# Optimization experiments

Measured on AMD Instinct MI355X. Metric: run time of the kernel, lower is better.

## Reference

```python
import jax, jax.numpy as jnp
import numpy as np

WS = 7   # window_size
SS = 3   # shift_size = window_size // 2
NH = 16  # num_heads


def _rel_pos_index(ws):
    coords = np.stack(np.meshgrid(np.arange(ws), np.arange(ws), indexing='ij'))  # (2, ws, ws)
    cf = coords.reshape(2, -1)
    rel = (cf[:, :, None] - cf[:, None, :]).transpose(1, 2, 0)
    rel[:, :, 0] += ws - 1
    rel[:, :, 1] += ws - 1
    rel[:, :, 0] *= 2 * ws - 1
    return rel.sum(-1)  # (ws*ws, ws*ws) int

REL_IDX = _rel_pos_index(WS)


def _attn_mask(h, w, ws, ss):
    img = np.zeros((h, w))
    sls = (slice(0, -ws), slice(-ws, -ss), slice(-ss, None))
    cnt = 0
    for i in sls:
        for j in sls:
            img[i, j] = cnt
            cnt += 1
    mw = img.reshape(h // ws, ws, w // ws, ws).transpose(0, 2, 1, 3).reshape(-1, ws * ws)
    d = mw[:, None, :] - mw[:, :, None]  # (nW, N, N)
    return np.where(d != 0, -100.0, 0.0).astype(np.float32)


def _part(x, ws):
    b, h, w, c = x.shape
    return x.reshape(b, h // ws, ws, w // ws, ws, c).transpose(0, 1, 3, 2, 4, 5).reshape(-1, ws * ws, c)


def _rev(win, ws, h, w):
    c = win.shape[-1]
    b = win.shape[0] // ((h // ws) * (w // ws))
    return win.reshape(b, h // ws, w // ws, ws, ws, c).transpose(0, 1, 3, 2, 4, 5).reshape(b, h, w, c)


def _ln(x, g, b):
    m = x.mean(-1, keepdims=True)
    v = x.var(-1, keepdims=True)
    return (x - m) / jnp.sqrt(v + 1e-5) * g + b


def _wattn(x, qkv_w, qkv_b, proj_w, proj_b, table, mask):
    B_, N, C = x.shape
    hd = C // NH
    scale = hd ** -0.5
    qkv = (x @ qkv_w.T + qkv_b).reshape(B_, N, 3, NH, hd).transpose(2, 0, 3, 1, 4)
    q, k, v = qkv[0] * scale, qkv[1], qkv[2]  # (B_, NH, N, hd)
    attn = jnp.einsum('bhnd,bhmd->bhnm', q, k)
    bias = table[REL_IDX.reshape(-1)].reshape(N, N, NH).transpose(2, 0, 1)  # (NH, N, N)
    attn = attn + bias[None]
    if mask is not None:
        nW = mask.shape[0]
        attn = (attn.reshape(B_ // nW, nW, NH, N, N) + mask[None, :, None]).reshape(B_, NH, N, N)
    attn = jax.nn.softmax(attn, axis=-1)
    out = jnp.einsum('bhnm,bhmd->bhnd', attn, v).transpose(0, 2, 1, 3).reshape(B_, N, C)
    return out @ proj_w.T + proj_b


def _mlp(x, w1, b1, w2, b2):
    return jax.nn.gelu(x @ w1.T + b1, approximate=False) @ w2.T + b2


def _forward(x, w_norm1_g, w_norm1_b, w_qkv_w, w_qkv_b, w_proj_w, w_proj_b, w_table,
             w_norm2_g, w_norm2_b, w_fc1_w, w_fc1_b, w_fc2_w, w_fc2_b,
             sw_norm1_g, sw_norm1_b, sw_qkv_w, sw_qkv_b, sw_proj_w, sw_proj_b, sw_table,
             sw_norm2_g, sw_norm2_b, sw_fc1_w, sw_fc1_b, sw_fc2_w, sw_fc2_b):
    b, c, h, w = x.shape
    x = jnp.transpose(x, (0, 2, 3, 1)).reshape(b, h * w, c)  # (B, HW, C)
    shortcut = x
    xn = _ln(x, w_norm1_g, w_norm1_b).reshape(b, h, w, c)
    aw = _wattn(_part(xn, WS), w_qkv_w, w_qkv_b, w_proj_w, w_proj_b, w_table, None)
    x = shortcut + _rev(aw, WS, h, w).reshape(b, h * w, c)
    x = x + _mlp(_ln(x, w_norm2_g, w_norm2_b), w_fc1_w, w_fc1_b, w_fc2_w, w_fc2_b)
    # shifted-window branch (shift_size > 0 since min(h,w) > window_size)
    xn = _ln(x, sw_norm1_g, sw_norm1_b)
    mask = jnp.asarray(_attn_mask(h, w, WS, SS))
    shifted = jnp.roll(xn.reshape(b, h, w, c), (-SS, -SS), axis=(1, 2))
    sa = _wattn(_part(shifted, WS), sw_qkv_w, sw_qkv_b, sw_proj_w, sw_proj_b, sw_table, mask)
    shifted = jnp.roll(_rev(sa, WS, h, w), (SS, SS), axis=(1, 2)).reshape(b, h * w, c)
    # NOTE: source adds the residual to the *normalized* activations here; kept faithful.
    x = xn + shifted
    x = x + _mlp(_ln(x, sw_norm2_g, sw_norm2_b), sw_fc1_w, sw_fc1_b, sw_fc2_w, sw_fc2_b)
    return x.reshape(b, h, w, c)


def setup_inputs() -> dict:
    key = jax.random.key(0)
    ks = jax.random.split(key, 32)
    B, C, H, W = 8, 512, 56, 56
    Cm = 4 * C
    T = (2 * WS - 1) ** 2

    def rn(k, shape, s=0.02):
        return jax.random.normal(k, shape, jnp.float32) * s

    d = {'x': jax.random.normal(ks[0], (B, C, H, W), jnp.float32)}
    for i, p in enumerate(['w', 'sw']):
        o = 1 + i * 6
        d[p + '_norm1_g'] = jnp.ones((C,), jnp.float32)
        d[p + '_norm1_b'] = jnp.zeros((C,), jnp.float32)
        d[p + '_qkv_w'] = rn(ks[o], (3 * C, C))
        d[p + '_qkv_b'] = jnp.zeros((3 * C,), jnp.float32)
        d[p + '_proj_w'] = rn(ks[o + 1], (C, C))
        d[p + '_proj_b'] = jnp.zeros((C,), jnp.float32)
        d[p + '_table'] = rn(ks[o + 2], (T, NH))
        d[p + '_norm2_g'] = jnp.ones((C,), jnp.float32)
        d[p + '_norm2_b'] = jnp.zeros((C,), jnp.float32)
        d[p + '_fc1_w'] = rn(ks[o + 3], (Cm, C))
        d[p + '_fc1_b'] = jnp.zeros((Cm,), jnp.float32)
        d[p + '_fc2_w'] = rn(ks[o + 4], (C, Cm))
        d[p + '_fc2_b'] = jnp.zeros((C,), jnp.float32)
    return d


def reference(x, w_norm1_g, w_norm1_b, w_qkv_w, w_qkv_b, w_proj_w, w_proj_b, w_table,
              w_norm2_g, w_norm2_b, w_fc1_w, w_fc1_b, w_fc2_w, w_fc2_b,
              sw_norm1_g, sw_norm1_b, sw_qkv_w, sw_qkv_b, sw_proj_w, sw_proj_b, sw_table,
              sw_norm2_g, sw_norm2_b, sw_fc1_w, sw_fc1_b, sw_fc2_w, sw_fc2_b):
    return _forward(x, w_norm1_g, w_norm1_b, w_qkv_w, w_qkv_b, w_proj_w, w_proj_b, w_table,
                    w_norm2_g, w_norm2_b, w_fc1_w, w_fc1_b, w_fc2_w, w_fc2_b,
                    sw_norm1_g, sw_norm1_b, sw_qkv_w, sw_qkv_b, sw_proj_w, sw_proj_b, sw_table,
                    sw_norm2_g, sw_norm2_b, sw_fc1_w, sw_fc1_b, sw_fc2_w, sw_fc2_b)
```

## Files before the change

### kernel.cpp

```cpp
#include <hip/hip_runtime.h>
#include <hip/hip_bf16.h>

using bf16 = __hip_bfloat16;

#define B_      8
#define C_      512
#define H_      56
#define W_      56
#define HW_     3136
#define M_      25088
#define NH_     16
#define HD_     32
#define WS_     7
#define NT_     49

typedef __attribute__((ext_vector_type(8))) short bf16x8;
typedef __attribute__((ext_vector_type(4))) float f32x4;

#define AS1(p) ((const __attribute__((address_space(1))) void*)(p))
#define AS3(p) ((__attribute__((address_space(3))) void*)(p))

__device__ inline float bf2f(const bf16 v) {
    unsigned short u = *reinterpret_cast<const unsigned short*>(&v);
    return __uint_as_float((unsigned)u << 16);
}
__device__ inline unsigned short f2bfu(float f) {
    bf16 h = __float2bfloat16(f);
    return *reinterpret_cast<unsigned short*>(&h);
}
__device__ inline float rdv(const float* p) { return *p; }
__device__ inline float rdv(const bf16* p)  { return bf2f(*p); }
__device__ inline void stv(float* p, float v) { *p = v; }
__device__ inline void stv(bf16* p, float v)  { *p = __float2bfloat16(v); }

__device__ inline float gelu_t(float v) {
    const float u = v * (0.79788456080286536f + 0.035677408136300125f * v * v);
    const float e = __expf(2.0f * u);
    return 0.5f * v * (2.0f - 2.0f / (e + 1.0f));
}

__global__ void k_detect(const void* g1, int* flag) {
    const unsigned short* u = (const unsigned short*)g1;
    *flag = (u[0] == 0x3F80u) ? 1 : 0;
}

struct WArgs {
    const void* src[26];
    bf16*       dst[26];
    int         n[26];
};
__global__ __launch_bounds__(256) void k_convert_all(WArgs a, const int* flag) {
    const int isb = *flag;
    const int gid = blockIdx.x * 256 + threadIdx.x;
    const int stride = gridDim.x * 256;
    #pragma unroll 1
    for (int w = 0; w < 26; ++w) {
        const int n = a.n[w];
        bf16* d = a.dst[w];
        if (isb) {
            const unsigned short* s = (const unsigned short*)a.src[w];
            for (int i = gid; i < n; i += stride) ((unsigned short*)d)[i] = s[i];
        } else {
            const float* s = (const float*)a.src[w];
            for (int i = gid; i < n; i += stride) d[i] = __float2bfloat16(s[i]);
        }
    }
}

__global__ __launch_bounds__(256) void k_transpose_in(const void* xin, bf16* X,
                                                      const int* flag) {
    __shared__ float tile[32][33];
    const int isb = *flag;
    const int p0 = blockIdx.x * 32, c0 = blockIdx.y * 32, b = blockIdx.z;
    const int tp = threadIdx.x & 31, tc = threadIdx.x >> 5;
    const size_t ibase = (size_t)b * C_ * HW_;
    #pragma unroll
    for (int i = 0; i < 4; ++i) {
        const int c = tc + i * 8;
        const size_t idx = ibase + (size_t)(c0 + c) * HW_ + p0 + tp;
        tile[c][tp] = isb ? bf2f(((const bf16*)xin)[idx]) : ((const float*)xin)[idx];
    }
    __syncthreads();
    const int wc = threadIdx.x & 31, wp = threadIdx.x >> 5;
    bf16* dst = X + (size_t)b * HW_ * C_;
    #pragma unroll
    for (int i = 0; i < 4; ++i) {
        const int p = wp + i * 8;
        dst[(size_t)(p0 + p) * C_ + c0 + wc] = __float2bfloat16(tile[wc][p]);
    }
}

__global__ __launch_bounds__(128) void k_layernorm(const bf16* __restrict__ X,
                                                   const bf16* __restrict__ g,
                                                   const bf16* __restrict__ bta,
                                                   bf16* __restrict__ XN) {
    const int tok = blockIdx.x;
    const ushort4 u = reinterpret_cast<const ushort4*>(X + (size_t)tok * C_)[threadIdx.x];
    float4 v;
    v.x = __uint_as_float((unsigned)u.x << 16);
    v.y = __uint_as_float((unsigned)u.y << 16);
    v.z = __uint_as_float((unsigned)u.z << 16);
    v.w = __uint_as_float((unsigned)u.w << 16);
    float s  = v.x + v.y + v.z + v.w;
    float s2 = v.x * v.x + v.y * v.y + v.z * v.z + v.w * v.w;
    #pragma unroll
    for (int o = 32; o > 0; o >>= 1) { s += __shfl_down(s, o); s2 += __shfl_down(s2, o); }
    __shared__ float sh[4];
    if ((threadIdx.x & 63) == 0) { sh[threadIdx.x >> 6] = s; sh[2 + (threadIdx.x >> 6)] = s2; }
    __syncthreads();
    const float ts = sh[0] + sh[1], ts2 = sh[2] + sh[3];
    const float m = ts * (1.0f / C_);
    const float var = ts2 * (1.0f / C_) - m * m;
    const float r = rsqrtf(var + 1e-5f);
    const int c = threadIdx.x * 4;
    ushort4 o;
    o.x = f2bfu((v.x - m) * r * bf2f(g[c + 0]) + bf2f(bta[c + 0]));
    o.y = f2bfu((v.y - m) * r * bf2f(g[c + 1]) + bf2f(bta[c + 1]));
    o.z = f2bfu((v.z - m) * r * bf2f(g[c + 2]) + bf2f(bta[c + 2]));
    o.w = f2bfu((v.w - m) * r * bf2f(g[c + 3]) + bf2f(bta[c + 3]));
    reinterpret_cast<ushort4*>(XN + (size_t)tok * C_)[threadIdx.x] = o;
}

template <typename TADD, typename TO, bool GELU, bool ADD, bool FINAL>
__global__ __launch_bounds__(512, 2) void k_gemm_mfma(const bf16* __restrict__ A,
                                                      const bf16* __restrict__ Wt,
                                                      const bf16* __restrict__ bias,
                                                      const TADD* __restrict__ addp,
                                                      TO* __restrict__ out,
                                                      const int* flag,
                                                      int N, int K) {
    __shared__ bf16 sA[3][256 * 64];
    __shared__ bf16 sB[3][128 * 64];
    const int tid  = threadIdx.x;
    const int lane = tid & 63;
    const int wid  = tid >> 6;
    const int wr   = wid >> 1;
    const int wc2  = wid & 1;

    const int nwg  = gridDim.x;
    const int orig = blockIdx.x;
    const int nx = nwg >> 3, rr_ = nwg & 7;
    const int xcd = orig & 7, offw = orig >> 3;
    const int wg = (xcd < rr_ ? xcd * (nx + 1) : rr_ * (nx + 1) + (xcd - rr_) * nx) + offw;
    const int gx = N >> 7;
    const int m0 = (wg / gx) * 256, n0 = (wg % gx) * 128;

    const f32x4 vz = {0.f, 0.f, 0.f, 0.f};
    f32x4 acc[4][4];
    #pragma unroll
    for (int i = 0; i < 4; ++i)
        #pragma unroll
        for (int j = 0; j < 4; ++j) acc[i][j] = vz;

    const int sr8  = lane >> 3;
    const int schk = (lane & 7) ^ sr8;
    const bf16* gA0 = A  + (size_t)(m0 + sr8) * K + schk * 8;
    const bf16* gB0 = Wt + (size_t)(n0 + sr8) * K + schk * 8;

    const int l15 = lane & 15, g4 = lane >> 4;
    const int NTLE = K >> 6;

    #pragma unroll
    for (int tt = 0; tt < 3; ++tt) {
        const int kt = tt << 6;
        #pragma unroll
        for (int p = 0; p < 4; ++p) {
            const int q = wid * 4 + p;
            __builtin_amdgcn_global_load_lds(AS1(gA0 + (size_t)(q * 8) * K + kt),
                                             AS3(&sA[tt][q * 512]), 16, 0, 0);
        }
        #pragma unroll
        for (int p = 0; p < 2; ++p) {
            const int q = wid * 2 + p;
            __builtin_amdgcn_global_load_lds(AS1(gB0 + (size_t)(q * 8) * K + kt),
                                             AS3(&sB[tt][q * 512]), 16, 0, 0);
        }
    }

    for (int t = 0; t < NTLE; ++t) {
        const int rem = NTLE - 1 - t;
        if (rem >= 2)      asm volatile("s_waitcnt vmcnt(12)" ::: "memory");
        else if (rem == 1) asm volatile("s_waitcnt vmcnt(6)"  ::: "memory");
        else               asm volatile("s_waitcnt vmcnt(0)"  ::: "memory");
        __builtin_amdgcn_s_barrier();

        const int buf = t % 3;
        bf16x8 bfr[4][2];
        #pragma unroll
        for (int ks = 0; ks < 2; ++ks) {
            const int ch = ((ks << 2) | g4) ^ (l15 & 7);
            #pragma unroll
            for (int j = 0; j < 4; ++j) {
                const int rowB = wc2 * 64 + j * 16 + l15;
                bfr[j][ks] = *reinterpret_cast<const bf16x8*>(&sB[buf][rowB * 64 + ch * 8]);
            }
        }
        const int ch0 = g4 ^ (l15 & 7);
        const int ch1 = (4 | g4) ^ (l15 & 7);
        __builtin_amdgcn_s_setprio(1);
        #pragma unroll
        for (int i = 0; i < 4; ++i) {
            const int rowA = wr * 64 + i * 16 + l15;
            const bf16x8 a0 = *reinterpret_cast<const bf16x8*>(&sA[buf][rowA * 64 + ch0 * 8]);
            const bf16x8 a1 = *reinterpret_cast<const bf16x8*>(&sA[buf][rowA * 64 + ch1 * 8]);
            #pragma unroll
            for (int j = 0; j < 4; ++j) {
                acc[i][j] = __builtin_amdgcn_mfma_f32_16x16x32_bf16(a0, bfr[j][0], acc[i][j], 0, 0, 0);
                acc[i][j] = __builtin_amdgcn_mfma_f32_16x16x32_bf16(a1, bfr[j][1], acc[i][j], 0, 0, 0);
            }
        }
        __builtin_amdgcn_s_setprio(0);

        asm volatile("s_waitcnt lgkmcnt(0)" ::: "memory");
        __builtin_amdgcn_s_barrier();

        const int tn = t + 3;
        if (tn < NTLE) {
            const int kt = tn << 6;
            #pragma unroll
            for (int p = 0; p < 4; ++p) {
                const int q = wid * 4 + p;
                __builtin_amdgcn_global_load_lds(AS1(gA0 + (size_t)(q * 8) * K + kt),
                                                 AS3(&sA[buf][q * 512]), 16, 0, 0);
            }
            #pragma unroll
            for (int p = 0; p < 2; ++p) {
                const int q = wid * 2 + p;
                __builtin_amdgcn_global_load_lds(AS1(gB0 + (size_t)(q * 8) * K + kt),
                                                 AS3(&sB[buf][q * 512]), 16, 0, 0);
            }
        }
    }

    int obf = 0;
    if constexpr (FINAL) obf = *flag;
    const int colBase = n0 + wc2 * 64 + l15;
    const int rowTop  = m0 + wr * 64 + g4 * 4;
    float bc[4];
    #pragma unroll
    for (int j = 0; j < 4; ++j) bc[j] = bf2f(bias[colBase + j * 16]);
    #pragma unroll
    for (int i = 0; i < 4; ++i) {
        #pragma unroll
        for (int r = 0; r < 4; ++r) {
            const int row = rowTop + i * 16 + r;
            #pragma unroll
            for (int j = 0; j < 4; ++j) {
                const int col = colBase + j * 16;
                float v = acc[i][j][r] + bc[j];
                if constexpr (GELU) v = gelu_t(v);
                if constexpr (ADD)  v += rdv(&addp[(size_t)row * N + col]);
                if constexpr (FINAL) {
                    if (obf) ((bf16*)(void*)out)[(size_t)row * N + col] = __float2bfloat16(v);
                    else     ((float*)(void*)out)[(size_t)row * N + col] = v;
                } else {
                    stv(&out[(size_t)row * N + col], v);
                }
            }
        }
    }
}

__global__ __launch_bounds__(256) void k_mktbl(const bf16* __restrict__ table,
                                               bf16* __restrict__ out, int shifted) {
    const int bh = blockIdx.x;
    const int cls = bh >> 4, h = bh & 15;
    const int rowE = shifted ? (cls >> 1) : 0;
    const int colE = shifted ? (cls & 1) : 0;
    for (int e = threadIdx.x; e < 64 * 64; e += 256) {
        const int i = e >> 6, j = e & 63;
        float v;
        if (i < NT_ && j < NT_) {
            const int yi = i / WS_, xi = i % WS_, yj = j / WS_, xj = j % WS_;
            const int ridx = (yi - yj + 6) * 13 + (xi - xj + 6);
            v = bf2f(table[ridx * NH_ + h]);
            const int ri = (rowE ? (yi < 4 ? 1 : 2) : 0) * 3 + (colE ? (xi < 4 ? 1 : 2) : 0);
            const int rj = (rowE ? (yj < 4 ? 1 : 2) : 0) * 3 + (colE ? (xj < 4 ? 1 : 2) : 0);
            if (ri != rj) v -= 100.f;
        } else if (j >= NT_) {
            v = -3e30f;
        } else {
            v = 0.f;
        }
        out[((size_t)bh << 12) + e] = __float2bfloat16(v);
    }
}

template <int SS, bool SHIFTED>
__global__ __launch_bounds__(64) void k_attn_mfma(const bf16* __restrict__ QKV,
                                                  const bf16* __restrict__ tbl,
                                                  bf16* __restrict__ O) {
    __shared__ __align__(16) short uQK[5120];
    __shared__ __align__(16) short uVt[2304];
    __shared__ int toks[NT_];
    short* Qs = uQK;
    short* Ks = uQK + 2560;
    short* Ps = uQK;

    const int lane = threadIdx.x;
    const int head = blockIdx.x & 15;
    const int win  = blockIdx.x >> 4;
    const int bl = win >> 6, w64 = win & 63;
    const int wy = w64 >> 3, wx = w64 & 7;

    if (lane < NT_) {
        const int dy = lane / WS_, dx = lane % WS_;
        const int sr = wy * WS_ + dy, scn = wx * WS_ + dx;
        const int r = (sr + SS) % H_, c = (scn + SS) % W_;
        toks[lane] = bl * HW_ + r * W_ + c;
    }
    __syncthreads();

    const int g4 = lane >> 4, l15 = lane & 15;
    const int tsg = lane >> 2, csg = (lane & 3) * 8;

    #pragma unroll
    for (int rr = 0; rr < 4; ++rr) {
        const int t = rr * 16 + tsg;
        bf16x8 qv = {0,0,0,0,0,0,0,0}, kv = {0,0,0,0,0,0,0,0}, vv = {0,0,0,0,0,0,0,0};
        if (t < NT_) {
            const bf16* base = QKV + (size_t)toks[t] * 1536 + head * HD_ + csg;
            qv = *reinterpret_cast<const bf16x8*>(base);
            kv = *reinterpret_cast<const bf16x8*>(base + 512);
            vv = *reinterpret_cast<const bf16x8*>(base + 1024);
        }
        *reinterpret_cast<bf16x8*>(&Qs[t * 40 + csg]) = qv;
        *reinterpret_cast<bf16x8*>(&Ks[t * 40 + csg]) = kv;
        #pragma unroll
        for (int e = 0; e < 8; ++e) uVt[(csg + e) * 72 + t] = ((const short*)&vv)[e];
    }
    __syncthreads();

    bf16x8 aq[4], bk[4];
    #pragma unroll
    for (int f = 0; f < 4; ++f) {
        aq[f] = *reinterpret_cast<const bf16x8*>(&Qs[(f * 16 + l15) * 40 + g4 * 8]);
        bk[f] = *reinterpret_cast<const bf16x8*>(&Ks[(f * 16 + l15) * 40 + g4 * 8]);
    }
    const f32x4 vz = {0.f, 0.f, 0.f, 0.f};
    f32x4 sacc[4][4];
    #pragma unroll
    for (int qi = 0; qi < 4; ++qi)
        #pragma unroll
        for (int kj = 0; kj < 4; ++kj)
            sacc[qi][kj] = __builtin_amdgcn_mfma_f32_16x16x32_bf16(aq[qi], bk[kj], vz, 0, 0, 0);
    __syncthreads();

    const int cls = SHIFTED ? (((wy == 7) ? 2 : 0) + ((wx == 7) ? 1 : 0)) : 0;
    const bf16* tb = tbl + (((size_t)(cls * NH_ + head)) << 12);
    const float scale = 0.17677669529663687f;
    #pragma unroll
    for (int qi = 0; qi < 4; ++qi) {
        #pragma unroll
        for (int r = 0; r < 4; ++r) {
            const int i = qi * 16 + g4 * 4 + r;
            const bf16* trow = tb + (i << 6);
            float sv[4];
            #pragma unroll
            for (int kj = 0; kj < 4; ++kj)
                sv[kj] = sacc[qi][kj][r] * scale + bf2f(trow[kj * 16 + l15]);
            float mx = fmaxf(fmaxf(sv[0], sv[1]), fmaxf(sv[2], sv[3]));
            #pragma unroll
            for (int d = 1; d <= 8; d <<= 1) mx = fmaxf(mx, __shfl_xor(mx, d));
            float p[4], sum = 0.f;
            #pragma unroll
            for (int kj = 0; kj < 4; ++kj) { p[kj] = __expf(sv[kj] - mx); sum += p[kj]; }
            #pragma unroll
            for (int d = 1; d <= 8; d <<= 1) sum += __shfl_xor(sum, d);
            const float inv = 1.0f / sum;
            #pragma unroll
            for (int kj = 0; kj < 4; ++kj)
                Ps[i * 72 + kj * 16 + l15] = (short)f2bfu(p[kj] * inv);
        }
    }
    __syncthreads();

    f32x4 oacc[4][2];
    #pragma unroll
    for (int qi = 0; qi < 4; ++qi) { oacc[qi][0] = vz; oacc[qi][1] = vz; }
    #pragma unroll
    for (int ks = 0; ks < 2; ++ks) {
        bf16x8 bv[2];
        #pragma unroll
        for (int dj = 0; dj < 2; ++dj)
            bv[dj] = *reinterpret_cast<const bf16x8*>(&uVt[(dj * 16 + l15) * 72 + ks * 32 + g4 * 8]);
        #pragma unroll
        for (int qi = 0; qi < 4; ++qi) {
            const bf16x8 ap = *reinterpret_cast<const bf16x8*>(&Ps[(qi * 16 + l15) * 72 + ks * 32 + g4 * 8]);
            #pragma unroll
            for (int dj = 0; dj < 2; ++dj)
                oacc[qi][dj] = __builtin_amdgcn_mfma_f32_16x16x32_bf16(ap, bv[dj], oacc[qi][dj], 0, 0, 0);
        }
    }
    #pragma unroll
    for (int qi = 0; qi < 4; ++qi) {
        #pragma unroll
        for (int r = 0; r < 4; ++r) {
            const int i = qi * 16 + g4 * 4 + r;
            if (i < NT_) {
                const size_t ob = (size_t)toks[i] * C_ + head * HD_ + l15;
                O[ob]      = __float2bfloat16(oacc[qi][0][r]);
                O[ob + 16] = __float2bfloat16(oacc[qi][1][r]);
            }
        }
    }
}

extern "C" void kernel_launch(void* const* d_in, const int* in_sizes, int n_in,
                              void* d_out, int out_size, void* d_ws, size_t ws_size,
                              hipStream_t stream) {
    (void)out_size; (void)ws_size;
    char* ws = (char*)d_ws;
    const size_t WEIGHT_RESERVE = 12651520;
    bf16*  WC   = (bf16*)ws;
    int*   FLG  = (int*)(ws + WEIGHT_RESERVE);
    bf16*  TBL1 = (bf16*)(ws + WEIGHT_RESERVE + 1024);
    bf16*  TBL2 = (bf16*)(ws + WEIGHT_RESERVE + 1024 + 131072);
    bf16*  X    = (bf16*)(ws + WEIGHT_RESERVE + 656384);
    bf16*  XN   = X + (size_t)M_ * C_;
    char*  BIG  = (char*)(XN + (size_t)M_ * C_);

    size_t offs[27];
    size_t off = 0;
    for (int i = 1; i < n_in && i < 27; ++i) { offs[i] = off; off += (size_t)((in_sizes[i] + 7) & ~7); }
    auto wc = [&](int i) { return (const bf16*)(WC + offs[i]); };

    k_detect<<<1, 1, 0, stream>>>(d_in[1], FLG);
    {
        WArgs a;
        for (int i = 1; i < 27; ++i) {
            a.src[i - 1] = d_in[i];
            a.dst[i - 1] = WC + offs[i];
            a.n[i - 1]   = in_sizes[i];
        }
        k_convert_all<<<512, 256, 0, stream>>>(a, FLG);
    }
    k_mktbl<<<16, 256, 0, stream>>>(wc(7),  TBL1, 0);
    k_mktbl<<<64, 256, 0, stream>>>(wc(20), TBL2, 1);

    const dim3 gT(HW_ / 32, C_ / 32, B_);
    k_transpose_in<<<gT, 256, 0, stream>>>(d_in[0], X, FLG);

    bf16* QKV = (bf16*)BIG;
    bf16* ATT = (bf16*)(BIG + (size_t)M_ * 1536 * 2);
    bf16* HID = (bf16*)BIG;

    const int gQ = (1536 / 128) * (M_ / 256);
    const int gP = (512 / 128)  * (M_ / 256);
    const int gF = (2048 / 128) * (M_ / 256);
    const dim3 gA(B_ * 64 * NH_);

    k_layernorm<<<M_, 128, 0, stream>>>(X, wc(1), wc(2), XN);
    k_gemm_mfma<bf16, bf16, false, false, false><<<gQ, 512, 0, stream>>>(
        XN, wc(3), wc(4), (const bf16*)nullptr, QKV, nullptr, 1536, C_);
    k_attn_mfma<0, false><<<gA, 64, 0, stream>>>(QKV, TBL1, ATT);
    k_gemm_mfma<bf16, bf16, false, true, false><<<gP, 512, 0, stream>>>(
        ATT, wc(5), wc(6), X, X, nullptr, C_, C_);
    k_layernorm<<<M_, 128, 0, stream>>>(X, wc(8), wc(9), XN);
    k_gemm_mfma<bf16, bf16, true, false, false><<<gF, 512, 0, stream>>>(
        XN, wc(10), wc(11), (const bf16*)nullptr, HID, nullptr, 2048, C_);
    k_gemm_mfma<bf16, bf16, false, true, false><<<gP, 512, 0, stream>>>(
        HID, wc(12), wc(13), X, X, nullptr, C_, 2048);
    k_layernorm<<<M_, 128, 0, stream>>>(X, wc(14), wc(15), XN);
    k_gemm_mfma<bf16, bf16, false, false, false><<<gQ, 512, 0, stream>>>(
        XN, wc(16), wc(17), (const bf16*)nullptr, QKV, nullptr, 1536, C_);
    k_attn_mfma<3, true><<<gA, 64, 0, stream>>>(QKV, TBL2, ATT);
    k_gemm_mfma<bf16, bf16, false, true, false><<<gP, 512, 0, stream>>>(
        ATT, wc(18), wc(19), XN, X, nullptr, C_, C_);
    k_layernorm<<<M_, 128, 0, stream>>>(X, wc(21), wc(22), XN);
    k_gemm_mfma<bf16, bf16, true, false, false><<<gF, 512, 0, stream>>>(
        XN, wc(23), wc(24), (const bf16*)nullptr, HID, nullptr, 2048, C_);
    k_gemm_mfma<bf16, float, false, true, true><<<gP, 512, 0, stream>>>(
        HID, wc(25), wc(26), X, (float*)d_out, FLG, C_, 2048);
}
```

Measured before the change: 849.3 us.

## Add 256x256-tile MFMA GEMM with XCD-aware block remap for QKV and MLP

Adds a new GEMM kernel that computes 256x256 output tiles with 8 waves, double-buffered half-tiles loaded straight into LDS, interleaved prefetch across the k-loop, and setprio around the MFMA bursts. Workgroup ids are remapped so consecutive tiles land on the same XCD, which should improve L2 reuse. The kernel replaces the older 256x128 GEMM for the QKV, FC1 and FC2 projections, raising arithmetic intensity per loaded byte. The cost is more registers and LDS per block and fewer blocks for the N=512 GEMMs, which may hurt occupancy or load balance.

```diff
diff --git a/kernel.cpp b/kernel.cpp
--- a/kernel.cpp
+++ b/kernel.cpp
@@ -119,6 +119,168 @@
     o.z = f2bfu((v.z - m) * r * bf2f(g[c + 2]) + bf2f(bta[c + 2]));
     o.w = f2bfu((v.w - m) * r * bf2f(g[c + 3]) + bf2f(bta[c + 3]));
     reinterpret_cast<ushort4*>(XN + (size_t)tok * C_)[threadIdx.x] = o;
+}
+
+template <typename TADD, typename TO, bool GELU, bool ADD, bool FINAL>
+__global__ __launch_bounds__(512, 2) void k_gemm8(const bf16* __restrict__ A,
+                                                  const bf16* __restrict__ Wt,
+                                                  const bf16* __restrict__ bias,
+                                                  const TADD* __restrict__ addp,
+                                                  TO* __restrict__ out,
+                                                  const int* flag,
+                                                  int N, int K) {
+    __shared__ bf16 sA[2][2][128 * 64];
+    __shared__ bf16 sB[2][2][128 * 64];
+    const int tid  = threadIdx.x;
+    const int lane = tid & 63;
+    const int wid  = tid >> 6;
+    const int wr   = wid >> 2;
+    const int wc2  = wid & 3;
+    const int bh   = wc2 >> 1;
+    const int brl  = (wc2 & 1) * 64;
+
+    const int nwg  = gridDim.x;
+    const int orig = blockIdx.x;
+    const int nx = nwg >> 3, rr_ = nwg & 7;
+    const int xcd = orig & 7, offw = orig >> 3;
+    const int wg = (xcd < rr_ ? xcd * (nx + 1) : rr_ * (nx + 1) + (xcd - rr_) * nx) + offw;
+    const int gx = N >> 8;
+    const int m0 = (wg / gx) * 256, n0 = (wg % gx) * 256;
+
+    const f32x4 vz = {0.f, 0.f, 0.f, 0.f};
+    f32x4 acc[8][4];
+    #pragma unroll
+    for (int i = 0; i < 8; ++i)
+        #pragma unroll
+        for (int j = 0; j < 4; ++j) acc[i][j] = vz;
+
+    const int sr8  = lane >> 3;
+    const int schk = (lane & 7) ^ sr8;
+    const bf16* gA0 = A  + (size_t)(m0 + sr8) * K + schk * 8;
+    const bf16* gB0 = Wt + (size_t)(n0 + sr8) * K + schk * 8;
+
+    const int l15 = lane & 15, g4 = lane >> 4;
+    const int NTL = K >> 6;
+    const int NITER = NTL >> 1;
+
+    auto stageA = [&](int d, int h, int T) {
+        const int kt = T << 6;
+        #pragma unroll
+        for (int p = 0; p < 2; ++p) {
+            const int q = wid * 2 + p;
+            __builtin_amdgcn_global_load_lds(
+                AS1(gA0 + (size_t)(h * 128 + q * 8) * K + kt),
+                AS3(&sA[d][h][q * 512]), 16, 0, 0);
+        }
+    };
+    auto stageB = [&](int d, int h, int T) {
+        const int kt = T << 6;
+        #pragma unroll
+        for (int p = 0; p < 2; ++p) {
+            const int q = wid * 2 + p;
+            __builtin_amdgcn_global_load_lds(
+                AS1(gB0 + (size_t)(h * 128 + q * 8) * K + kt),
+                AS3(&sB[d][h][q * 512]), 16, 0, 0);
+        }
+    };
+
+    stageA(0, 0, 0); stageA(0, 1, 0);
+    stageB(0, 0, 0); stageB(0, 1, 0);
+    stageB(1, 0, 1); stageB(1, 1, 1);
+    asm volatile("s_waitcnt vmcnt(4)" ::: "memory");
+    __builtin_amdgcn_s_barrier();
+
+    #pragma unroll 1
+    for (int it = 0; it < NITER; ++it) {
+        const bool nl = (it < NITER - 1);
+        #pragma unroll
+        for (int half = 0; half < 2; ++half) {
+            bf16x8 bfr[4][2];
+            #pragma unroll
+            for (int q = 0; q < 4; ++q) {
+                if (q == 0) {
+                    #pragma unroll
+                    for (int ks = 0; ks < 2; ++ks) {
+                        const int ch = ((ks << 2) | g4) ^ (l15 & 7);
+                        #pragma unroll
+                        for (int j = 0; j < 4; ++j) {
+                            const int r = brl + j * 16 + l15;
+                            bfr[j][ks] = *reinterpret_cast<const bf16x8*>(&sB[half][bh][r * 64 + ch * 8]);
+                        }
+                    }
+                }
+                bf16x8 af[2][2];
+                #pragma unroll
+                for (int ks = 0; ks < 2; ++ks) {
+                    const int ch = ((ks << 2) | g4) ^ (l15 & 7);
+                    #pragma unroll
+                    for (int ii = 0; ii < 2; ++ii) {
+                        const int r = (q * 2 + ii) * 16 + l15;
+                        af[ii][ks] = *reinterpret_cast<const bf16x8*>(&sA[half][wr][r * 64 + ch * 8]);
+                    }
+                }
+                if (half == 0) {
+                    if (q == 0)            { stageA(1, 0, 2 * it + 1); stageA(1, 1, 2 * it + 1); }
+                    else if (q == 1 && nl) { stageB(0, 0, 2 * it + 2); }
+                    else if (q == 2 && nl) { stageB(0, 1, 2 * it + 2); }
+                } else {
+                    if (q == 0 && nl)      { stageA(0, 0, 2 * it + 2); }
+                    else if (q == 1 && nl) { stageA(0, 1, 2 * it + 2); }
+                    else if (q == 2 && nl) { stageB(1, 0, 2 * it + 3); }
+                    else if (q == 3 && nl) { stageB(1, 1, 2 * it + 3); }
+                }
+                __builtin_amdgcn_s_barrier();
+                asm volatile("s_waitcnt lgkmcnt(0)" ::: "memory");
+                __builtin_amdgcn_s_setprio(1);
+                #pragma unroll
+                for (int ks = 0; ks < 2; ++ks)
+                    #pragma unroll
+                    for (int ii = 0; ii < 2; ++ii)
+                        #pragma unroll
+                        for (int j = 0; j < 4; ++j)
+                            acc[q * 2 + ii][j] = __builtin_amdgcn_mfma_f32_16x16x32_bf16(
+                                af[ii][ks], bfr[j][ks], acc[q * 2 + ii][j], 0, 0, 0);
+                __builtin_amdgcn_s_setprio(0);
+                if (q == 3) {
+                    if (half == 0) {
+                        if (nl) asm volatile("s_waitcnt vmcnt(4)" ::: "memory");
+                        else    asm volatile("s_waitcnt vmcnt(0)" ::: "memory");
+                    } else if (nl) {
+                        asm volatile("s_waitcnt vmcnt(4)" ::: "memory");
+                    }
+                }
+                __builtin_amdgcn_s_barrier();
+            }
+        }
+    }
+
+    int obf = 0;
+    if constexpr (FINAL) obf = *flag;
+    const int colBase = n0 + wc2 * 64 + l15;
+    const int rowTop  = m0 + wr * 128 + g4 * 4;
+    float bc[4];
+    #pragma unroll
+    for (int j = 0; j < 4; ++j) bc[j] = bf2f(bias[colBase + j * 16]);
+    #pragma unroll
+    for (int i = 0; i < 8; ++i) {
+        #pragma unroll
+        for (int r = 0; r < 4; ++r) {
+            const int row = rowTop + i * 16 + r;
+            #pragma unroll
+            for (int j = 0; j < 4; ++j) {
+                const int col = colBase + j * 16;
+                float v = acc[i][j][r] + bc[j];
+                if constexpr (GELU) v = gelu_t(v);
+                if constexpr (ADD)  v += rdv(&addp[(size_t)row * N + col]);
+                if constexpr (FINAL) {
+                    if (obf) ((bf16*)(void*)out)[(size_t)row * N + col] = __float2bfloat16(v);
+                    else     ((float*)(void*)out)[(size_t)row * N + col] = v;
+                } else {
+                    stv(&out[(size_t)row * N + col], v);
+                }
+            }
+        }
+    }
 }
 
 template <typename TADD, typename TO, bool GELU, bool ADD, bool FINAL>
@@ -445,31 +607,32 @@
     bf16* ATT = (bf16*)(BIG + (size_t)M_ * 1536 * 2);
     bf16* HID = (bf16*)BIG;
 
-    const int gQ = (1536 / 128) * (M_ / 256);
+    const int gQ = (1536 / 256) * (M_ / 256);
+    const int gF = (2048 / 256) * (M_ / 256);
     const int gP = (512 / 128)  * (M_ / 256);
-    const int gF = (2048 / 128) * (M_ / 256);
+    const int gO = (512 / 256)  * (M_ / 256);
     const dim3 gA(B_ * 64 * NH_);
 
     k_layernorm<<<M_, 128, 0, stream>>>(X, wc(1), wc(2), XN);
-    k_gemm_mfma<bf16, bf16, false, false, false><<<gQ, 512, 0, stream>>>(
+    k_gemm8<bf16, bf16, false, false, false><<<gQ, 512, 0, stream>>>(
         XN, wc(3), wc(4), (const bf16*)nullptr, QKV, nullptr, 1536, C_);
     k_attn_mfma<0, false><<<gA, 64, 0, stream>>>(QKV, TBL1, ATT);
     k_gemm_mfma<bf16, bf16, false, true, false><<<gP, 512, 0, stream>>>(
         ATT, wc(5), wc(6), X, X, nullptr, C_, C_);
     k_layernorm<<<M_, 128, 0, stream>>>(X, wc(8), wc(9), XN);
-    k_gemm_mfma<bf16, bf16, true, false, false><<<gF, 512, 0, stream>>>(
+    k_gemm8<bf16, bf16, true, false, false><<<gF, 512, 0, stream>>>(
         XN, wc(10), wc(11), (const bf16*)nullptr, HID, nullptr, 2048, C_);
-    k_gemm_mfma<bf16, bf16, false, true, false><<<gP, 512, 0, stream>>>(
+    k_gemm8<bf16, bf16, false, true, false><<<gO, 512, 0, stream>>>(
         HID, wc(12), wc(13), X, X, nullptr, C_, 2048);
     k_layernorm<<<M_, 128, 0, stream>>>(X, wc(14), wc(15), XN);
-    k_gemm_mfma<bf16, bf16, false, false, false><<<gQ, 512, 0, stream>>>(
+    k_gemm8<bf16, bf16, false, false, false><<<gQ, 512, 0, stream>>>(
         XN, wc(16), wc(17), (const bf16*)nullptr, QKV, nullptr, 1536, C_);
     k_attn_mfma<3, true><<<gA, 64, 0, stream>>>(QKV, TBL2, ATT);
     k_gemm_mfma<bf16, bf16, false, true, false><<<gP, 512, 0, stream>>>(
         ATT, wc(18), wc(19), XN, X, nullptr, C_, C_);
     k_layernorm<<<M_, 128, 0, stream>>>(X, wc(21), wc(22), XN);
-    k_gemm_mfma<bf16, bf16, true, false, false><<<gF, 512, 0, stream>>>(
+    k_gemm8<bf16, bf16, true, false, false><<<gF, 512, 0, stream>>>(
         XN, wc(23), wc(24), (const bf16*)nullptr, HID, nullptr, 2048, C_);
-    k_gemm_mfma<bf16, float, false, true, true><<<gP, 512, 0, stream>>>(
+    k_gemm8<bf16, float, false, true, true><<<gO, 512, 0, stream>>>(
         HID, wc(25), wc(26), X, (float*)d_out, FLG, C_, 2048);
 }
```

Result: faster. 794.6 us, median of 2 (-6.4%).
